# Kernel tuning notes

Measured on AMD Instinct MI355X. Metric: run time of the kernel, lower is better.

## Reference

```python
import jax, jax.numpy as jnp
import numpy as np

B, S, D, H = 2, 4096, 512, 8
HD = D // H


def setup_inputs() -> dict:
    key = jax.random.key(0)
    ks = jax.random.split(key, 6)
    scale = 1.0 / np.sqrt(D)
    return {
        "inputs": jax.random.normal(ks[0], (B, S, D), jnp.float32),
        "Wq": jax.random.normal(ks[1], (D, D), jnp.float32) * scale,
        "bq": jnp.zeros((D,), jnp.float32),
        "Wk": jax.random.normal(ks[2], (D, D), jnp.float32) * scale,
        "bk": jnp.zeros((D,), jnp.float32),
        "Wv": jax.random.normal(ks[3], (D, D), jnp.float32) * scale,
        "bv": jnp.zeros((D,), jnp.float32),
        "Wo": jax.random.normal(ks[4], (D, D), jnp.float32) * scale,
        "bo": jnp.zeros((D,), jnp.float32),
    }


def reference(inputs, Wq, bq, Wk, bk, Wv, bv, Wo, bo):
    # QKV projections: [B,S,D]
    q = inputs @ Wq + bq
    k = inputs @ Wk + bk
    v = inputs @ Wv + bv

    def split_heads(x):  # [B,S,D] -> [B,H,S,hd]
        return x.reshape(B, S, H, HD).transpose(0, 2, 1, 3)

    q, k, v = split_heads(q), split_heads(k), split_heads(v)

    # scaled dot-product attention, softmax over last axis
    scores = jnp.einsum("bhsd,bhtd->bhst", q, k) / jnp.sqrt(jnp.float32(HD))
    weights = jax.nn.softmax(scores, axis=-1)
    attn = jnp.einsum("bhst,bhtd->bhsd", weights, v)  # [B,H,S,hd]

    # merge heads and output projection
    attn = attn.transpose(0, 2, 1, 3).reshape(B, S, D)
    return attn @ Wo + bo
```

## Files before the change

### kernel.cpp

```cpp
#include <hip/hip_runtime.h>

#define BATCH 2
#define S_LEN 4096
#define D_MODEL 512
#define N_HEAD 8
#define HEAD_D 64

typedef _Float16 f16;
typedef _Float16 half8 __attribute__((ext_vector_type(8)));
typedef _Float16 half4v __attribute__((ext_vector_type(4)));
typedef float f32x2 __attribute__((ext_vector_type(2)));
typedef float f32x4 __attribute__((ext_vector_type(4)));
typedef float f32x16 __attribute__((ext_vector_type(16)));
typedef float float4v __attribute__((ext_vector_type(4)));
typedef unsigned int uint2v __attribute__((ext_vector_type(2)));
typedef unsigned int uint4v __attribute__((ext_vector_type(4)));

#define AS1(p) ((const __attribute__((address_space(1))) unsigned int*)(p))
#define AS3(p) ((__attribute__((address_space(3))) unsigned int*)(p))

__device__ __forceinline__ f32x4 zero4() {
    f32x4 z; z[0] = 0.f; z[1] = 0.f; z[2] = 0.f; z[3] = 0.f; return z;
}

__device__ __forceinline__ unsigned pkh(float a, float b) {
    auto v = __builtin_amdgcn_cvt_pkrtz(a, b);
    return __builtin_bit_cast(unsigned, v);
}

__device__ __forceinline__ float fexp2(float x) {
    return __builtin_amdgcn_exp2f(x);
}

__global__ __launch_bounds__(256) void cvt_kernel(const float* __restrict__ X,
                                                  const float* __restrict__ Wq,
                                                  const float* __restrict__ Wk,
                                                  const float* __restrict__ Wv,
                                                  const float* __restrict__ Wo,
                                                  f16* __restrict__ X16,
                                                  f16* __restrict__ Wt) {
    int b = blockIdx.x;
    if (b < 4096) {
        int i = (b * 256 + threadIdx.x) * 4;
        float4v v = *(const float4v*)(X + i);
        half4v h;
        h[0] = (f16)v[0]; h[1] = (f16)v[1]; h[2] = (f16)v[2]; h[3] = (f16)v[3];
        *(half4v*)(X16 + i) = h;
    } else {
        int bb = b - 4096;
        int by = bb >> 10, bx = bb & 1023;
        const float* src = (by == 0) ? Wq : (by == 1) ? Wk : (by == 2) ? Wv : Wo;
        int idx = bx * 256 + threadIdx.x;
        int n = idx >> 9, k = idx & 511;
        Wt[(size_t)by * 262144 + idx] = (f16)src[k * 512 + n];
    }
}

template<int BN>
__device__ __forceinline__ void gemm_core(const f16* __restrict__ A,
                                          const f16* __restrict__ Bt,
                                          int m0, int n0, int K,
                                          f16* ldsA, f16* ldsB,
                                          f32x4 (&acc)[4][BN / 32]) {
    constexpr int FN = BN / 32;
    const int t = threadIdx.x;
    const int lane = t & 63;
    const int w = t >> 6;
    const int g = lane >> 4, r = lane & 15;
    const int wm = (w >> 1) * 64, wn = (w & 1) * (BN / 2);

    #pragma unroll
    for (int i = 0; i < 4; ++i)
        #pragma unroll
        for (int j = 0; j < FN; ++j) acc[i][j] = zero4();

    for (int k0 = 0; k0 < K; k0 += 32) {
        __syncthreads();
        #pragma unroll
        for (int it = 0; it < 2; ++it) {
            int s = t + 256 * it;
            int row = s >> 2, c8s = s & 3;
            int c8d = c8s ^ ((row >> 1) & 3);
            __builtin_amdgcn_global_load_lds(AS1(A + (size_t)(m0 + row) * K + k0 + c8d * 8),
                                             AS3(ldsA + s * 8), 16, 0, 0);
        }
        #pragma unroll
        for (int it = 0; it < BN / 64; ++it) {
            int s = t + 256 * it;
            int row = s >> 2, c8s = s & 3;
            int c8d = c8s ^ ((row >> 1) & 3);
            __builtin_amdgcn_global_load_lds(AS1(Bt + (size_t)(n0 + row) * K + k0 + c8d * 8),
                                             AS3(ldsB + s * 8), 16, 0, 0);
        }
        __syncthreads();
        half8 af[4], bf[FN];
        #pragma unroll
        for (int fm = 0; fm < 4; ++fm) {
            int row = wm + fm * 16 + r;
            af[fm] = *(const half8*)(ldsA + row * 32 + (g ^ ((row >> 1) & 3)) * 8);
        }
        #pragma unroll
        for (int fn = 0; fn < FN; ++fn) {
            int row = wn + fn * 16 + r;
            bf[fn] = *(const half8*)(ldsB + row * 32 + (g ^ ((row >> 1) & 3)) * 8);
        }
        #pragma unroll
        for (int fm = 0; fm < 4; ++fm)
            #pragma unroll
            for (int fn = 0; fn < FN; ++fn)
                acc[fm][fn] = __builtin_amdgcn_mfma_f32_16x16x32_f16(af[fm], bf[fn],
                                                                     acc[fm][fn], 0, 0, 0);
    }
}

#define QSCALE 0.18033688011112042f

__global__ __launch_bounds__(256) void gemm_qkv_kernel(const f16* __restrict__ X16,
                                                       const f16* __restrict__ Wt,
                                                       const float* __restrict__ bq,
                                                       const float* __restrict__ bk,
                                                       const float* __restrict__ bv,
                                                       f16* __restrict__ Q16,
                                                       f16* __restrict__ K16,
                                                       f16* __restrict__ Vt) {
    __shared__ f16 ldsA[128 * 32];
    __shared__ f16 ldsB[128 * 32];
    const int z = blockIdx.z;
    const f16* Bt = Wt + (size_t)z * 262144;
    const float* bias = (z == 0) ? bq : (z == 1) ? bk : bv;
    const int m0 = blockIdx.y * 128, n0 = blockIdx.x * 128;

    f32x4 acc[4][4];
    gemm_core<128>(X16, Bt, m0, n0, 512, ldsA, ldsB, acc);

    const int lane = threadIdx.x & 63, w = threadIdx.x >> 6;
    const int g = lane >> 4, r = lane & 15;
    const int wm = (w >> 1) * 64, wn = (w & 1) * 64;

    if (z == 2) {
        #pragma unroll
        for (int fm = 0; fm < 4; ++fm) {
            #pragma unroll
            for (int fn = 0; fn < 4; ++fn) {
                int col = n0 + wn + fn * 16 + r;
                float bcol = bias[col];
                int row0 = m0 + wm + fm * 16 + g * 4;
                f16* dst = Vt + ((size_t)((row0 >> 12) * N_HEAD + (col >> 6)) * HEAD_D
                                 + (col & 63)) * S_LEN + (row0 & 4095);
                half4v ph;
                #pragma unroll
                for (int i = 0; i < 4; ++i) ph[i] = (f16)(acc[fm][fn][i] + bcol);
                *(half4v*)dst = ph;
            }
        }
    } else {
        f16* out = (z == 0) ? Q16 : K16;
        const float scale = (z == 0) ? QSCALE : 1.0f;
        #pragma unroll
        for (int fm = 0; fm < 4; ++fm) {
            #pragma unroll
            for (int fn = 0; fn < 4; ++fn) {
                int col = n0 + wn + fn * 16 + r;
                float bcol = bias[col];
                #pragma unroll
                for (int i = 0; i < 4; ++i) {
                    int row = m0 + wm + fm * 16 + g * 4 + i;
                    out[(size_t)row * 512 + col] = (f16)((acc[fm][fn][i] + bcol) * scale);
                }
            }
        }
    }
}

__global__ __launch_bounds__(256) void gemm_out_kernel(const f16* __restrict__ A16,
                                                       const f16* __restrict__ Wot,
                                                       const float* __restrict__ bo,
                                                       float* __restrict__ out) {
    __shared__ f16 ldsA[128 * 32];
    __shared__ f16 ldsB[64 * 32];
    const int m0 = blockIdx.y * 128, n0 = blockIdx.x * 64;

    f32x4 acc[4][2];
    gemm_core<64>(A16, Wot, m0, n0, 512, ldsA, ldsB, acc);

    const int lane = threadIdx.x & 63, w = threadIdx.x >> 6;
    const int g = lane >> 4, r = lane & 15;
    const int wm = (w >> 1) * 64, wn = (w & 1) * 32;
    #pragma unroll
    for (int fm = 0; fm < 4; ++fm) {
        #pragma unroll
        for (int fn = 0; fn < 2; ++fn) {
            int col = n0 + wn + fn * 16 + r;
            float bcol = bo[col];
            #pragma unroll
            for (int i = 0; i < 4; ++i) {
                int row = m0 + wm + fm * 16 + g * 4 + i;
                out[(size_t)row * 512 + col] = acc[fm][fn][i] + bcol;
            }
        }
    }
}

template<int NSPLIT>
__global__ __launch_bounds__(256, 4) void attn_kernel(const f16* __restrict__ Q16,
                                                      const f16* __restrict__ K16,
                                                      const f16* __restrict__ Vt,
                                                      f16* __restrict__ A16,
                                                      f16* __restrict__ Opart,
                                                      float* __restrict__ lpart) {
    __shared__ f16 kl[4 * 2048];
    __shared__ f16 vl[4 * 2048];

    const int t = threadIdx.x;
    const int lane = t & 63, w = t >> 6;
    const int li = lane & 31, hh = lane >> 5;

    constexpr int TOTALB = 512 * NSPLIT;
    int flat = blockIdx.x + (blockIdx.y << 5) + blockIdx.z * 512;
    int lf = (flat & 7) * (TOTALB >> 3) + (flat >> 3);
    const int qi = lf & 31;
    const int bh = (lf >> 5) & 15;
    const int split = lf >> 9;
    const int qb = qi * 128;
    const int b = bh >> 3, h = bh & 7;
    const size_t hb = (size_t)b * S_LEN * D_MODEL + h * HEAD_D;
    const f16* Vh = Vt + (size_t)bh * HEAD_D * S_LEN;
    constexpr int NT = 128 / NSPLIT;
    static_assert(NT % 4 == 0, "loop processes 4 tiles per iteration");
    const int kv0 = split * (S_LEN / NSPLIT);

    const int srow = t >> 3;
    const int c8d = (t & 7) ^ ((srow & 7) ^ (srow >> 3));
    const f16* kp = K16 + hb + (size_t)(kv0 + srow) * D_MODEL + c8d * 8;
    const int srow_v = t >> 2;
    const int c4d = (t & 3) ^ (((srow_v & 7) ^ (srow_v >> 3)) & 3);
    const f16* vp = Vh + (size_t)srow_v * S_LEN + kv0 + c4d * 8;

    half8 qf[4];
    const f16* qptr = Q16 + hb + (size_t)(qb + w * 32 + li) * D_MODEL + hh * 8;
    #pragma unroll
    for (int c = 0; c < 4; ++c) qf[c] = *(const half8*)(qptr + c * 16);

    const int fr8 = (li & 7) ^ (li >> 3);
    const int fv4 = fr8 & 3;
    int koff[4], voff[2][2];
    #pragma unroll
    for (int c = 0; c < 4; ++c)
        koff[c] = li * 64 + ((((2 * c + hh) ^ fr8) & 7) * 8);
    #pragma unroll
    for (int i = 0; i < 2; ++i)
        #pragma unroll
        for (int c = 0; c < 2; ++c)
            voff[i][c] = (i * 32 + li) * 32 + ((((2 * c + hh) ^ fv4) & 3) * 8);

    f32x16 o[2];
    #pragma unroll
    for (int i = 0; i < 16; ++i) { o[0][i] = 0.f; o[1][i] = 0.f; }
    f32x2 ls2; ls2[0] = 0.f; ls2[1] = 0.f;

    auto compute = [&](const f16* kb, const f16* vb) {
        f32x16 sA;
        #pragma unroll
        for (int i = 0; i < 16; ++i) sA[i] = 0.f;
        __builtin_amdgcn_s_setprio(1);
        #pragma unroll
        for (int c = 0; c < 4; ++c) {
            half8 k0 = *(const half8*)(kb + koff[c]);
            sA = __builtin_amdgcn_mfma_f32_32x32x16_f16(k0, qf[c], sA, 0, 0, 0);
        }
        __builtin_amdgcn_s_setprio(0);
        asm volatile("" : "+v"(sA));

        #pragma unroll
        for (int c = 0; c < 2; ++c) {
            unsigned W[4];
            #pragma unroll
            for (int m4 = 0; m4 < 4; ++m4) {
                int mm = c * 4 + m4;
                float a0 = fexp2(sA[2 * mm]), a1 = fexp2(sA[2 * mm + 1]);
                f32x2 p2; p2[0] = a0; p2[1] = a1;
                ls2 += p2;
                W[m4] = pkh(a0, a1);
            }
            uint2v r0 = __builtin_amdgcn_permlane32_swap(W[0], W[2], false, false);
            W[0] = r0[0]; W[2] = r0[1];
            uint2v r1 = __builtin_amdgcn_permlane32_swap(W[1], W[3], false, false);
            W[1] = r1[0]; W[3] = r1[1];

            __builtin_amdgcn_s_setprio(1);
            uint4v u; u[0] = W[0]; u[1] = W[1]; u[2] = W[2]; u[3] = W[3];
            half8 pa = __builtin_bit_cast(half8, u);
            half8 v0 = *(const half8*)(vb + voff[0][c]);
            half8 v1 = *(const half8*)(vb + voff[1][c]);
            o[0] = __builtin_amdgcn_mfma_f32_32x32x16_f16(pa, v0, o[0], 0, 0, 0);
            o[1] = __builtin_amdgcn_mfma_f32_32x32x16_f16(pa, v1, o[1], 0, 0, 0);
            __builtin_amdgcn_s_setprio(0);
        }
    };

    __builtin_amdgcn_global_load_lds(AS1(kp), AS3(kl + t * 8), 16, 0, 0);
    __builtin_amdgcn_global_load_lds(AS1(vp), AS3(vl + t * 8), 16, 0, 0);
    kp += 32 * D_MODEL; vp += 32;
    __builtin_amdgcn_global_load_lds(AS1(kp), AS3(kl + 2048 + t * 8), 16, 0, 0);
    __builtin_amdgcn_global_load_lds(AS1(vp), AS3(vl + 2048 + t * 8), 16, 0, 0);
    __syncthreads();

    #pragma unroll 1
    for (int kt = 0; kt < NT / 4; ++kt) {
        kp += 32 * D_MODEL; vp += 32;
        __builtin_amdgcn_global_load_lds(AS1(kp), AS3(kl + 2 * 2048 + t * 8), 16, 0, 0);
        __builtin_amdgcn_global_load_lds(AS1(vp), AS3(vl + 2 * 2048 + t * 8), 16, 0, 0);
        kp += 32 * D_MODEL; vp += 32;
        __builtin_amdgcn_global_load_lds(AS1(kp), AS3(kl + 3 * 2048 + t * 8), 16, 0, 0);
        __builtin_amdgcn_global_load_lds(AS1(vp), AS3(vl + 3 * 2048 + t * 8), 16, 0, 0);
        compute(kl, vl);
        compute(kl + 2048, vl + 2048);
        __syncthreads();

        if (kt < NT / 4 - 1) {
            kp += 32 * D_MODEL; vp += 32;
            __builtin_amdgcn_global_load_lds(AS1(kp), AS3(kl + t * 8), 16, 0, 0);
            __builtin_amdgcn_global_load_lds(AS1(vp), AS3(vl + t * 8), 16, 0, 0);
            kp += 32 * D_MODEL; vp += 32;
            __builtin_amdgcn_global_load_lds(AS1(kp), AS3(kl + 2048 + t * 8), 16, 0, 0);
            __builtin_amdgcn_global_load_lds(AS1(vp), AS3(vl + 2048 + t * 8), 16, 0, 0);
        }
        compute(kl + 2 * 2048, vl + 2 * 2048);
        compute(kl + 3 * 2048, vl + 3 * 2048);
        __syncthreads();
    }

    float lsum = ls2[0] + ls2[1];
    float l2 = lsum + __shfl_xor(lsum, 32);

    if (NSPLIT == 1) {
        float rl = 1.0f / l2;
        #pragma unroll
        for (int r = 0; r < 16; ++r) {
            int qrow = (r & 3) + 8 * (r >> 2) + 4 * hh;
            float ri = __shfl(rl, qrow);
            f16* dst = A16 + hb + (size_t)(qb + w * 32 + qrow) * D_MODEL + li;
            dst[0]  = (f16)(o[0][r] * ri);
            dst[32] = (f16)(o[1][r] * ri);
        }
    } else {
        f16* op = Opart + ((size_t)(split * 16 + bh) * S_LEN + qb + w * 32) * HEAD_D;
        #pragma unroll
        for (int r = 0; r < 16; ++r) {
            int qrow = (r & 3) + 8 * (r >> 2) + 4 * hh;
            op[qrow * 64 + li]      = (f16)o[0][r];
            op[qrow * 64 + 32 + li] = (f16)o[1][r];
        }
        if (lane < 32)
            lpart[(size_t)(split * 16 + bh) * S_LEN + qb + w * 32 + lane] = l2;
    }
}

template<int NSPLIT>
__global__ __launch_bounds__(256) void combine_kernel(const f16* __restrict__ Opart,
                                                      const float* __restrict__ lpart,
                                                      f16* __restrict__ A16) {
    int idx = blockIdx.x * 256 + threadIdx.x;
    if (idx >= 524288) return;
    int hd8 = (idx & 7) * 8;
    int q = (idx >> 3) & 4095;
    int bh = idx >> 15;
    size_t base = ((size_t)bh * S_LEN + q) * HEAD_D + hd8;
    float acc[8];
    #pragma unroll
    for (int j = 0; j < 8; ++j) acc[j] = 0.f;
    float l = 0.f;
    #pragma unroll
    for (int s = 0; s < NSPLIT; ++s) {
        half8 a = *(const half8*)(Opart + (size_t)s * 4194304 + base);
        #pragma unroll
        for (int j = 0; j < 8; ++j) acc[j] += (float)a[j];
        l += lpart[(size_t)s * 65536 + (size_t)bh * S_LEN + q];
    }
    float rl = 1.0f / l;
    half8 r;
    #pragma unroll
    for (int j = 0; j < 8; ++j) r[j] = (f16)(acc[j] * rl);
    int bb = bh >> 3, hh = bh & 7;
    *(half8*)(A16 + ((size_t)bb * S_LEN + q) * D_MODEL + hh * 64 + hd8) = r;
}

extern "C" void kernel_launch(void* const* d_in, const int* in_sizes, int n_in,
                              void* d_out, int out_size, void* d_ws, size_t ws_size,
                              hipStream_t stream) {
    const float* X  = (const float*)d_in[0];
    const float* Wq = (const float*)d_in[1];
    const float* bq = (const float*)d_in[2];
    const float* Wk = (const float*)d_in[3];
    const float* bk = (const float*)d_in[4];
    const float* Wv = (const float*)d_in[5];
    const float* bv = (const float*)d_in[6];
    const float* Wo = (const float*)d_in[7];
    const float* bo = (const float*)d_in[8];

    f16* ws    = (f16*)d_ws;
    f16* X16   = ws;
    f16* Wt    = X16 + 4194304;
    f16* Q16   = Wt + 1048576;
    f16* K16   = Q16 + 4194304;
    f16* Vt    = K16 + 4194304;
    f16* Opart = Vt + 4194304;
    f16* A16   = X16;

    const int nsplit = (ws_size >= 52953088ull) ? 2 : 1;

    cvt_kernel<<<dim3(8192), dim3(256), 0, stream>>>(X, Wq, Wk, Wv, Wo, X16, Wt);
    gemm_qkv_kernel<<<dim3(4, 64, 3), dim3(256), 0, stream>>>(X16, Wt, bq, bk, bv,
                                                              Q16, K16, Vt);
    if (nsplit == 2) {
        float* lp2 = (float*)(Opart + 8388608);
        attn_kernel<2><<<dim3(32, 16, 2), dim3(256), 0, stream>>>(Q16, K16, Vt, A16,
                                                                  Opart, lp2);
        combine_kernel<2><<<dim3(2048), dim3(256), 0, stream>>>(Opart, lp2, A16);
    } else {
        float* lp1 = (float*)(Opart + 4194304);
        attn_kernel<1><<<dim3(32, 16, 1), dim3(256), 0, stream>>>(Q16, K16, Vt, A16,
                                                                  Opart, lp1);
    }
    gemm_out_kernel<<<dim3(8, 64), dim3(256), 0, stream>>>(A16, Wt + 3 * 262144, bo,
                                                           (float*)d_out);
}
```

Baseline: 140.5 us.

## Fuse split-KV combine into output projection GEMM

Removes the separate combine kernel and instead merges the two split partial outputs and normalizes by the summed softmax denominators while loading the A tile of the output projection GEMM. This saves a launch and a round trip of the combined attention output through memory. The trade-off is that each of the 8 column-blocks re-reads and re-combines both Opart halves, so partial data is read 8x over with synchronous loads instead of async LDS loads. It also drops an asm barrier on the score accumulator in the attention kernel.

```diff
diff --git a/kernel.cpp b/kernel.cpp
--- a/kernel.cpp
+++ b/kernel.cpp
@@ -201,6 +201,111 @@
     }
 }
 
+__global__ __launch_bounds__(256) void gemm_out_fused(const f16* __restrict__ Opart,
+                                                      const float* __restrict__ lpart,
+                                                      const f16* __restrict__ Wot,
+                                                      const float* __restrict__ bo,
+                                                      float* __restrict__ out) {
+    __shared__ f16 ldsA[128 * 32];
+    __shared__ f16 ldsB[64 * 32];
+    __shared__ float ldsRL[128 * 8];
+    const int m0 = blockIdx.y * 128, n0 = blockIdx.x * 64;
+    const int t = threadIdx.x;
+
+    const int bB = m0 >> 12;
+    const int q0 = m0 & 4095;
+    {
+        int hl = t >> 7;
+        int rr = t & 127;
+        #pragma unroll
+        for (int j = 0; j < 4; ++j) {
+            int h = hl + 2 * j;
+            size_t li = (size_t)(bB * 8 + h) * 4096 + q0 + rr;
+            float l = lpart[li] + lpart[65536 + li];
+            ldsRL[rr * 8 + h] = 1.0f / l;
+        }
+    }
+
+    f32x4 acc[4][2];
+    #pragma unroll
+    for (int i = 0; i < 4; ++i)
+        #pragma unroll
+        for (int j = 0; j < 2; ++j) acc[i][j] = zero4();
+
+    const int lane = t & 63;
+    const int w = t >> 6;
+    const int g = lane >> 4, r = lane & 15;
+    const int wm = (w >> 1) * 64, wn = (w & 1) * 32;
+
+    const int row_s0 = t >> 2;
+    const int c8d_0 = (t & 3) ^ ((row_s0 >> 1) & 3);
+    const int row_s1 = row_s0 + 64;
+    const int c8d_1 = (t & 3) ^ ((row_s1 >> 1) & 3);
+
+    for (int k0 = 0; k0 < 512; k0 += 32) {
+        __syncthreads();
+        const int h = k0 >> 6;
+        const int hd0 = k0 & 32;
+        #pragma unroll
+        for (int it = 0; it < 2; ++it) {
+            int s = t + 256 * it;
+            int row = it ? row_s1 : row_s0;
+            int c8d = it ? c8d_1 : c8d_0;
+            size_t base = ((size_t)(bB * 8 + h) * 4096 + q0 + row) * 64 + hd0 + c8d * 8;
+            half8 a0 = *(const half8*)(Opart + base);
+            half8 a1 = *(const half8*)(Opart + 4194304 + base);
+            float rl = ldsRL[row * 8 + h];
+            uint4v Wp;
+            #pragma unroll
+            for (int j = 0; j < 4; ++j) {
+                float x0 = ((float)a0[2 * j] + (float)a1[2 * j]) * rl;
+                float x1 = ((float)a0[2 * j + 1] + (float)a1[2 * j + 1]) * rl;
+                Wp[j] = pkh(x0, x1);
+            }
+            *(half8*)(ldsA + s * 8) = __builtin_bit_cast(half8, Wp);
+        }
+        {
+            int s = t;
+            int row = s >> 2, c8s = s & 3;
+            int c8d = c8s ^ ((row >> 1) & 3);
+            __builtin_amdgcn_global_load_lds(AS1(Wot + (size_t)(n0 + row) * 512 + k0 + c8d * 8),
+                                             AS3(ldsB + s * 8), 16, 0, 0);
+        }
+        __syncthreads();
+        half8 af[4], bf[2];
+        #pragma unroll
+        for (int fm = 0; fm < 4; ++fm) {
+            int row = wm + fm * 16 + r;
+            af[fm] = *(const half8*)(ldsA + row * 32 + (g ^ ((row >> 1) & 3)) * 8);
+        }
+        #pragma unroll
+        for (int fn = 0; fn < 2; ++fn) {
+            int row = wn + fn * 16 + r;
+            bf[fn] = *(const half8*)(ldsB + row * 32 + (g ^ ((row >> 1) & 3)) * 8);
+        }
+        #pragma unroll
+        for (int fm = 0; fm < 4; ++fm)
+            #pragma unroll
+            for (int fn = 0; fn < 2; ++fn)
+                acc[fm][fn] = __builtin_amdgcn_mfma_f32_16x16x32_f16(af[fm], bf[fn],
+                                                                     acc[fm][fn], 0, 0, 0);
+    }
+
+    #pragma unroll
+    for (int fm = 0; fm < 4; ++fm) {
+        #pragma unroll
+        for (int fn = 0; fn < 2; ++fn) {
+            int col = n0 + wn + fn * 16 + r;
+            float bcol = bo[col];
+            #pragma unroll
+            for (int i = 0; i < 4; ++i) {
+                int row = m0 + wm + fm * 16 + g * 4 + i;
+                out[(size_t)row * 512 + col] = acc[fm][fn][i] + bcol;
+            }
+        }
+    }
+}
+
 template<int NSPLIT>
 __global__ __launch_bounds__(256, 4) void attn_kernel(const f16* __restrict__ Q16,
                                                       const f16* __restrict__ K16,
@@ -269,7 +374,6 @@
             sA = __builtin_amdgcn_mfma_f32_32x32x16_f16(k0, qf[c], sA, 0, 0, 0);
         }
         __builtin_amdgcn_s_setprio(0);
-        asm volatile("" : "+v"(sA));
 
         #pragma unroll
         for (int c = 0; c < 2; ++c) {
@@ -354,35 +458,6 @@
         if (lane < 32)
             lpart[(size_t)(split * 16 + bh) * S_LEN + qb + w * 32 + lane] = l2;
     }
-}
-
-template<int NSPLIT>
-__global__ __launch_bounds__(256) void combine_kernel(const f16* __restrict__ Opart,
-                                                      const float* __restrict__ lpart,
-                                                      f16* __restrict__ A16) {
-    int idx = blockIdx.x * 256 + threadIdx.x;
-    if (idx >= 524288) return;
-    int hd8 = (idx & 7) * 8;
-    int q = (idx >> 3) & 4095;
-    int bh = idx >> 15;
-    size_t base = ((size_t)bh * S_LEN + q) * HEAD_D + hd8;
-    float acc[8];
-    #pragma unroll
-    for (int j = 0; j < 8; ++j) acc[j] = 0.f;
-    float l = 0.f;
-    #pragma unroll
-    for (int s = 0; s < NSPLIT; ++s) {
-        half8 a = *(const half8*)(Opart + (size_t)s * 4194304 + base);
-        #pragma unroll
-        for (int j = 0; j < 8; ++j) acc[j] += (float)a[j];
-        l += lpart[(size_t)s * 65536 + (size_t)bh * S_LEN + q];
-    }
-    float rl = 1.0f / l;
-    half8 r;
-    #pragma unroll
-    for (int j = 0; j < 8; ++j) r[j] = (f16)(acc[j] * rl);
-    int bb = bh >> 3, hh = bh & 7;
-    *(half8*)(A16 + ((size_t)bb * S_LEN + q) * D_MODEL + hh * 64 + hd8) = r;
 }
 
 extern "C" void kernel_launch(void* const* d_in, const int* in_sizes, int n_in,
@@ -416,12 +491,14 @@
         float* lp2 = (float*)(Opart + 8388608);
         attn_kernel<2><<<dim3(32, 16, 2), dim3(256), 0, stream>>>(Q16, K16, Vt, A16,
                                                                   Opart, lp2);
-        combine_kernel<2><<<dim3(2048), dim3(256), 0, stream>>>(Opart, lp2, A16);
+        gemm_out_fused<<<dim3(8, 64), dim3(256), 0, stream>>>(Opart, lp2,
+                                                              Wt + 3 * 262144, bo,
+                                                              (float*)d_out);
     } else {
         float* lp1 = (float*)(Opart + 4194304);
         attn_kernel<1><<<dim3(32, 16, 1), dim3(256), 0, stream>>>(Q16, K16, Vt, A16,
                                                                   Opart, lp1);
-    }
-    gemm_out_kernel<<<dim3(8, 64), dim3(256), 0, stream>>>(A16, Wt + 3 * 262144, bo,
-                                                           (float*)d_out);
-}
+        gemm_out_kernel<<<dim3(8, 64), dim3(256), 0, stream>>>(A16, Wt + 3 * 262144, bo,
+                                                               (float*)d_out);
+    }
+}
```

Result: no change. 143.1 us (+1.8%).

## Double-buffer GEMM LDS staging and transpose MFMA operands for vectorized epilogue stores

Applied to the files above, without the earlier changes.

The shared GEMM core now prefetches the next K-slice into a second LDS buffer while computing on the current one, dropping one barrier per iteration so global-to-LDS loads overlap with MFMA work. For the Q/K and output projections the MFMA operands are swapped, so each lane holds four consecutive columns of one row, which lets the epilogue use vector bias loads and vector stores instead of scalar strided stores. A compiler barrier on the attention score accumulator is also removed. LDS use per block doubles, which may reduce occupancy.

```diff
diff --git a/kernel.cpp b/kernel.cpp
--- a/kernel.cpp
+++ b/kernel.cpp
@@ -56,7 +56,7 @@
     }
 }
 
-template<int BN>
+template<int BN, bool SWAP>
 __device__ __forceinline__ void gemm_core(const f16* __restrict__ A,
                                           const f16* __restrict__ Bt,
                                           int m0, int n0, int K,
@@ -74,42 +74,63 @@
         #pragma unroll
         for (int j = 0; j < FN; ++j) acc[i][j] = zero4();
 
-    for (int k0 = 0; k0 < K; k0 += 32) {
-        __syncthreads();
+    auto stage = [&](int k0, int buf) {
+        f16* dA = ldsA + buf * (128 * 32);
         #pragma unroll
         for (int it = 0; it < 2; ++it) {
             int s = t + 256 * it;
             int row = s >> 2, c8s = s & 3;
             int c8d = c8s ^ ((row >> 1) & 3);
             __builtin_amdgcn_global_load_lds(AS1(A + (size_t)(m0 + row) * K + k0 + c8d * 8),
-                                             AS3(ldsA + s * 8), 16, 0, 0);
-        }
+                                             AS3(dA + s * 8), 16, 0, 0);
+        }
+        f16* dB = ldsB + buf * (BN * 32);
         #pragma unroll
         for (int it = 0; it < BN / 64; ++it) {
             int s = t + 256 * it;
             int row = s >> 2, c8s = s & 3;
             int c8d = c8s ^ ((row >> 1) & 3);
             __builtin_amdgcn_global_load_lds(AS1(Bt + (size_t)(n0 + row) * K + k0 + c8d * 8),
-                                             AS3(ldsB + s * 8), 16, 0, 0);
-        }
-        __syncthreads();
+                                             AS3(dB + s * 8), 16, 0, 0);
+        }
+    };
+
+    auto compute = [&](int buf) {
+        const f16* cA = ldsA + buf * (128 * 32);
+        const f16* cB = ldsB + buf * (BN * 32);
         half8 af[4], bf[FN];
         #pragma unroll
         for (int fm = 0; fm < 4; ++fm) {
             int row = wm + fm * 16 + r;
-            af[fm] = *(const half8*)(ldsA + row * 32 + (g ^ ((row >> 1) & 3)) * 8);
+            af[fm] = *(const half8*)(cA + row * 32 + (g ^ ((row >> 1) & 3)) * 8);
         }
         #pragma unroll
         for (int fn = 0; fn < FN; ++fn) {
             int row = wn + fn * 16 + r;
-            bf[fn] = *(const half8*)(ldsB + row * 32 + (g ^ ((row >> 1) & 3)) * 8);
+            bf[fn] = *(const half8*)(cB + row * 32 + (g ^ ((row >> 1) & 3)) * 8);
         }
         #pragma unroll
         for (int fm = 0; fm < 4; ++fm)
             #pragma unroll
-            for (int fn = 0; fn < FN; ++fn)
-                acc[fm][fn] = __builtin_amdgcn_mfma_f32_16x16x32_f16(af[fm], bf[fn],
-                                                                     acc[fm][fn], 0, 0, 0);
+            for (int fn = 0; fn < FN; ++fn) {
+                if (SWAP)
+                    acc[fm][fn] = __builtin_amdgcn_mfma_f32_16x16x32_f16(bf[fn], af[fm],
+                                                                         acc[fm][fn], 0, 0, 0);
+                else
+                    acc[fm][fn] = __builtin_amdgcn_mfma_f32_16x16x32_f16(af[fm], bf[fn],
+                                                                         acc[fm][fn], 0, 0, 0);
+            }
+    };
+
+    const int nk = K / 32;
+    stage(0, 0);
+    __syncthreads();
+    #pragma unroll 1
+    for (int ks = 0; ks < nk; ++ks) {
+        int cur = ks & 1;
+        if (ks + 1 < nk) stage((ks + 1) * 32, cur ^ 1);
+        compute(cur);
+        __syncthreads();
     }
 }
 
@@ -123,21 +144,20 @@
                                                        f16* __restrict__ Q16,
                                                        f16* __restrict__ K16,
                                                        f16* __restrict__ Vt) {
-    __shared__ f16 ldsA[128 * 32];
-    __shared__ f16 ldsB[128 * 32];
+    __shared__ f16 ldsA[2 * 128 * 32];
+    __shared__ f16 ldsB[2 * 128 * 32];
     const int z = blockIdx.z;
     const f16* Bt = Wt + (size_t)z * 262144;
     const float* bias = (z == 0) ? bq : (z == 1) ? bk : bv;
     const int m0 = blockIdx.y * 128, n0 = blockIdx.x * 128;
 
-    f32x4 acc[4][4];
-    gemm_core<128>(X16, Bt, m0, n0, 512, ldsA, ldsB, acc);
-
     const int lane = threadIdx.x & 63, w = threadIdx.x >> 6;
     const int g = lane >> 4, r = lane & 15;
     const int wm = (w >> 1) * 64, wn = (w & 1) * 64;
 
+    f32x4 acc[4][4];
     if (z == 2) {
+        gemm_core<128, false>(X16, Bt, m0, n0, 512, ldsA, ldsB, acc);
         #pragma unroll
         for (int fm = 0; fm < 4; ++fm) {
             #pragma unroll
@@ -154,19 +174,21 @@
             }
         }
     } else {
+        gemm_core<128, true>(X16, Bt, m0, n0, 512, ldsA, ldsB, acc);
         f16* out = (z == 0) ? Q16 : K16;
         const float scale = (z == 0) ? QSCALE : 1.0f;
         #pragma unroll
         for (int fm = 0; fm < 4; ++fm) {
+            int row = m0 + wm + fm * 16 + r;
             #pragma unroll
             for (int fn = 0; fn < 4; ++fn) {
-                int col = n0 + wn + fn * 16 + r;
-                float bcol = bias[col];
+                int colb = n0 + wn + fn * 16 + g * 4;
+                float4v b4 = *(const float4v*)(bias + colb);
+                half4v ph;
                 #pragma unroll
-                for (int i = 0; i < 4; ++i) {
-                    int row = m0 + wm + fm * 16 + g * 4 + i;
-                    out[(size_t)row * 512 + col] = (f16)((acc[fm][fn][i] + bcol) * scale);
-                }
+                for (int i = 0; i < 4; ++i)
+                    ph[i] = (f16)((acc[fm][fn][i] + b4[i]) * scale);
+                *(half4v*)(out + (size_t)row * 512 + colb) = ph;
             }
         }
     }
@@ -176,27 +198,27 @@
                                                        const f16* __restrict__ Wot,
                                                        const float* __restrict__ bo,
                                                        float* __restrict__ out) {
-    __shared__ f16 ldsA[128 * 32];
-    __shared__ f16 ldsB[64 * 32];
+    __shared__ f16 ldsA[2 * 128 * 32];
+    __shared__ f16 ldsB[2 * 64 * 32];
     const int m0 = blockIdx.y * 128, n0 = blockIdx.x * 64;
 
     f32x4 acc[4][2];
-    gemm_core<64>(A16, Wot, m0, n0, 512, ldsA, ldsB, acc);
+    gemm_core<64, true>(A16, Wot, m0, n0, 512, ldsA, ldsB, acc);
 
     const int lane = threadIdx.x & 63, w = threadIdx.x >> 6;
     const int g = lane >> 4, r = lane & 15;
     const int wm = (w >> 1) * 64, wn = (w & 1) * 32;
     #pragma unroll
     for (int fm = 0; fm < 4; ++fm) {
+        int row = m0 + wm + fm * 16 + r;
         #pragma unroll
         for (int fn = 0; fn < 2; ++fn) {
-            int col = n0 + wn + fn * 16 + r;
-            float bcol = bo[col];
+            int colb = n0 + wn + fn * 16 + g * 4;
+            float4v b4 = *(const float4v*)(bo + colb);
+            float4v o4;
             #pragma unroll
-            for (int i = 0; i < 4; ++i) {
-                int row = m0 + wm + fm * 16 + g * 4 + i;
-                out[(size_t)row * 512 + col] = acc[fm][fn][i] + bcol;
-            }
+            for (int i = 0; i < 4; ++i) o4[i] = acc[fm][fn][i] + b4[i];
+            *(float4v*)(out + (size_t)row * 512 + colb) = o4;
         }
     }
 }
@@ -269,7 +291,6 @@
             sA = __builtin_amdgcn_mfma_f32_32x32x16_f16(k0, qf[c], sA, 0, 0, 0);
         }
         __builtin_amdgcn_s_setprio(0);
-        asm volatile("" : "+v"(sA));
 
         #pragma unroll
         for (int c = 0; c < 2; ++c) {
```

Result: slower. 147.4 us (+4.9%).
